# Optimization experiments

Measured on AMD Instinct MI355X. Metric: run time of the kernel, lower is better.

## Reference

```python
import jax, jax.numpy as jnp
import numpy as np
import math

B, S, D_IN, D_Q = 4, 2048, 512, 512

def setup_inputs() -> dict:
    key = jax.random.key(0)
    ks = jax.random.split(key, 7)
    s_in = 1.0 / math.sqrt(D_IN)
    x = jax.random.normal(ks[0], (B, S, D_IN), dtype=jnp.float32)
    # nn.Linear-style params: W [out,in], b [out]; uniform(-1/sqrt(in), 1/sqrt(in))
    Wq = jax.random.uniform(ks[1], (D_Q, D_IN), jnp.float32, -s_in, s_in)
    bq = jax.random.uniform(ks[2], (D_Q,), jnp.float32, -s_in, s_in)
    Wk = jax.random.uniform(ks[3], (D_Q, D_IN), jnp.float32, -s_in, s_in)
    bk = jax.random.uniform(ks[4], (D_Q,), jnp.float32, -s_in, s_in)
    Wv = jax.random.uniform(ks[5], (D_Q, D_IN), jnp.float32, -s_in, s_in)
    bv = jax.random.uniform(ks[6], (D_Q,), jnp.float32, -s_in, s_in)
    return {"x": x, "Wq": Wq, "bq": bq, "Wk": Wk, "bk": bk, "Wv": Wv, "bv": bv}

def reference(x, Wq, bq, Wk, bk, Wv, bv):
    # Q/K/V projections: [B,S,D_IN] @ W^T + b -> [B,S,D_Q]
    Q = jnp.einsum('bsi,qi->bsq', x, Wq) + bq
    K = jnp.einsum('bsi,qi->bsq', x, Wk) + bk
    V = jnp.einsum('bsi,qi->bsq', x, Wv) + bv
    scale = 1.0 / math.sqrt(D_Q)
    scores = jnp.einsum('bsq,btq->bst', Q, K) * scale  # [B,S,S]
    attention = jax.nn.softmax(scores, axis=-1)        # 'atten_prob'
    weighted = jnp.einsum('bst,btq->bsq', attention, V)  # 'atten_score'
    return (attention, weighted)
```

## Files before the change

### kernel.cpp

```cpp
#include <hip/hip_runtime.h>
#include <hip/hip_bf16.h>

typedef unsigned short u16;
typedef short bf16x8 __attribute__((ext_vector_type(8)));
typedef float f32x4 __attribute__((ext_vector_type(4)));

#define S_LEN 2048
#define DQ 512
#define NBATCH 4

__device__ __forceinline__ u16 f2bf(float f) {
    __hip_bfloat16 h = __float2bfloat16(f);
    return *reinterpret_cast<u16*>(&h);
}
__device__ __forceinline__ float bf2f(u16 u) {
    unsigned v = ((unsigned)u) << 16;
    union { unsigned u; float f; } c; c.u = v; return c.f;
}

__device__ __forceinline__ void async16(const u16* g, u16* l) {
    __builtin_amdgcn_global_load_lds(
        (__attribute__((address_space(1))) void*)g,
        (__attribute__((address_space(3))) void*)l, 16, 0, 0);
}

__device__ __forceinline__ int xcd_swz(int bid, int chunk) {
    return (bid & 7) * chunk + (bid >> 3);
}

__global__ __launch_bounds__(256) void k_cvt_all(const float* __restrict__ x,
                                                 const float* __restrict__ wq,
                                                 const float* __restrict__ wk,
                                                 const float* __restrict__ wv,
                                                 u16* __restrict__ xb, u16* __restrict__ wb) {
    int bid = blockIdx.x;
    const float* src;
    u16* dst;
    int i;
    if (bid < 4096)      { src = x;  dst = xb;          i = bid * 256 + threadIdx.x; }
    else if (bid < 4352) { src = wq; dst = wb;          i = (bid - 4096) * 256 + threadIdx.x; }
    else if (bid < 4608) { src = wk; dst = wb + 262144; i = (bid - 4352) * 256 + threadIdx.x; }
    else                 { src = wv; dst = wb + 524288; i = (bid - 4608) * 256 + threadIdx.x; }
    f32x4 v = *(const f32x4*)(src + (size_t)i * 4);
    ushort4 o;
    o.x = f2bf(v.x); o.y = f2bf(v.y); o.z = f2bf(v.z); o.w = f2bf(v.w);
    *(ushort4*)(dst + (size_t)i * 4) = o;
}

__device__ __forceinline__ void gemm_core(const u16* __restrict__ A, const u16* __restrict__ B,
                                          int lda, int ldb, int kend,
                                          f32x4 acc[4][4], u16* ldsA, u16* ldsB, int tid) {
    const int lane = tid & 63;
    const int w    = tid >> 6;
    const int wm   = (w & 1) << 6;
    const int wn   = (w >> 1) << 6;
    const int l16  = lane & 15;
    const int quad = lane >> 4;

    for (int k0 = 0; k0 < kend; k0 += 32) {
#pragma unroll
        for (int i = 0; i < 2; ++i) {
            int c  = i * 256 + tid;
            int r  = c >> 2;
            int cc = (c & 3) << 3;
            async16(A + (size_t)r * lda + k0 + cc, ldsA + r * 32 + cc);
            async16(B + (size_t)r * ldb + k0 + cc, ldsB + r * 32 + cc);
        }
        __syncthreads();
        bf16x8 af[4], bf[4];
#pragma unroll
        for (int i = 0; i < 4; ++i)
            af[i] = *(const bf16x8*)(ldsA + (wm + i * 16 + l16) * 32 + quad * 8);
#pragma unroll
        for (int j = 0; j < 4; ++j)
            bf[j] = *(const bf16x8*)(ldsB + (wn + j * 16 + l16) * 32 + quad * 8);
#pragma unroll
        for (int i = 0; i < 4; ++i)
#pragma unroll
            for (int j = 0; j < 4; ++j)
                acc[i][j] = __builtin_amdgcn_mfma_f32_16x16x32_bf16(af[i], bf[j], acc[i][j], 0, 0, 0);
        __syncthreads();
    }
}

__global__ __launch_bounds__(256) void k_proj(const u16* __restrict__ xb, const u16* __restrict__ Wb,
                                              const float* __restrict__ bq, const float* __restrict__ bk,
                                              const float* __restrict__ bv, u16* __restrict__ out,
                                              u16* __restrict__ VT) {
    __shared__ __align__(16) u16 lds[8192];
    const int l  = xcd_swz(blockIdx.x, 96);
    const int bx = l & 3;
    const int by = (l >> 2) & 63;
    const int z  = l >> 8;
    const int m0 = by * 128, n0 = bx * 128;
    const u16* A = xb + (size_t)m0 * DQ;
    const u16* B = Wb + (size_t)z * DQ * DQ + (size_t)n0 * DQ;
    const float* bias = (z == 0) ? bq : (z == 1) ? bk : bv;

    f32x4 acc[4][4];
#pragma unroll
    for (int i = 0; i < 4; ++i)
#pragma unroll
        for (int j = 0; j < 4; ++j) acc[i][j] = (f32x4)0.0f;

    int tid = threadIdx.x;
    gemm_core(A, B, DQ, DQ, DQ, acc, lds, lds + 4096, tid);

    const int lane = tid & 63, w = tid >> 6;
    const int wm = (w & 1) << 6, wn = (w >> 1) << 6;
    const int l16 = lane & 15, quad = lane >> 4;

    if (z < 2) {
        u16* outz = out + (size_t)z * 8192 * DQ;
#pragma unroll
        for (int j = 0; j < 4; ++j) {
            int gn = n0 + wn + j * 16 + l16;
            float bb = bias[gn];
#pragma unroll
            for (int i = 0; i < 4; ++i)
#pragma unroll
                for (int r = 0; r < 4; ++r) {
                    int gm = m0 + wm + i * 16 + quad * 4 + r;
                    outz[(size_t)gm * DQ + gn] = f2bf(acc[i][j][r] + bb);
                }
        }
    } else {
        const int b = m0 >> 11;
        u16* VTb_ = VT + (size_t)b * DQ * S_LEN;
#pragma unroll
        for (int j = 0; j < 4; ++j) {
            int gn = n0 + wn + j * 16 + l16;
            float bb = bias[gn];
#pragma unroll
            for (int i = 0; i < 4; ++i) {
                int t0 = (m0 & 2047) + wm + i * 16 + quad * 4;
                ushort4 o;
                o.x = f2bf(acc[i][j][0] + bb);
                o.y = f2bf(acc[i][j][1] + bb);
                o.z = f2bf(acc[i][j][2] + bb);
                o.w = f2bf(acc[i][j][3] + bb);
                *(ushort4*)(VTb_ + (size_t)gn * S_LEN + t0) = o;
            }
        }
    }
}

__global__ __launch_bounds__(256) void k_scores(const u16* __restrict__ Qb, const u16* __restrict__ Kb,
                                                u16* __restrict__ Pb) {
    __shared__ __align__(16) u16 lds[8192];
    const int l  = xcd_swz(blockIdx.x, 128);
    const int bx = l & 15;
    const int by = (l >> 4) & 15;
    const int b  = l >> 8;
    const int m0 = by * 128, n0 = bx * 128;
    const u16* A = Qb + ((size_t)b * S_LEN + m0) * DQ;
    const u16* B = Kb + ((size_t)b * S_LEN + n0) * DQ;

    f32x4 acc[4][4];
#pragma unroll
    for (int i = 0; i < 4; ++i)
#pragma unroll
        for (int j = 0; j < 4; ++j) acc[i][j] = (f32x4)0.0f;

    int tid = threadIdx.x;
    gemm_core(A, B, DQ, DQ, DQ, acc, lds, lds + 4096, tid);

    const float scale = 0.044194173824159216f;
    const int lane = tid & 63, w = tid >> 6;
    const int wm = (w & 1) << 6, wn = (w >> 1) << 6;
    const int l16 = lane & 15, quad = lane >> 4;
    u16* prow = Pb + (size_t)(b * S_LEN + m0) * S_LEN;
#pragma unroll
    for (int i = 0; i < 4; ++i)
#pragma unroll
        for (int j = 0; j < 4; ++j)
#pragma unroll
            for (int r = 0; r < 4; ++r) {
                int gm = wm + i * 16 + quad * 4 + r;
                int gn = n0 + wn + j * 16 + l16;
                prow[(size_t)gm * S_LEN + gn] = f2bf(__expf(acc[i][j][r] * scale));
            }
}

__global__ __launch_bounds__(256) void k_norm(const u16* __restrict__ Pb,
                                              float* __restrict__ probs,
                                              float* __restrict__ inv_sums) {
    __shared__ float red[4];
    const int row = blockIdx.x;
    const u16* pr = Pb + (size_t)row * S_LEN;
    float* outr = probs + (size_t)row * S_LEN;
    const int tid = threadIdx.x, lane = tid & 63, w = tid >> 6;

    bf16x8 pv = *(const bf16x8*)(pr + (size_t)tid * 8);
    float f[8];
#pragma unroll
    for (int k = 0; k < 8; ++k) f[k] = bf2f((u16)pv[k]);

    float sum = ((f[0] + f[1]) + (f[2] + f[3])) + ((f[4] + f[5]) + (f[6] + f[7]));
#pragma unroll
    for (int off = 32; off > 0; off >>= 1) sum += __shfl_xor(sum, off);
    if (lane == 0) red[w] = sum;
    __syncthreads();
    sum = (red[0] + red[1]) + (red[2] + red[3]);
    float inv = 1.0f / sum;
    if (tid == 0) inv_sums[row] = inv;

    f32x4 o0, o1;
    o0.x = f[0] * inv; o0.y = f[1] * inv; o0.z = f[2] * inv; o0.w = f[3] * inv;
    o1.x = f[4] * inv; o1.y = f[5] * inv; o1.z = f[6] * inv; o1.w = f[7] * inv;
    *(f32x4*)(outr + (size_t)tid * 8) = o0;
    *(f32x4*)(outr + (size_t)tid * 8 + 4) = o1;
}

__global__ __launch_bounds__(256) void k_pv(const u16* __restrict__ Pb, const u16* __restrict__ VT,
                                            const float* __restrict__ inv_sums,
                                            float* __restrict__ wout) {
    __shared__ __align__(16) u16 lds[12288];
    u16* ldsA = lds;
    u16* ldsB = lds + 8192;
    const int l  = xcd_swz(blockIdx.x, 64);
    const int bx = l & 7;
    const int by = (l >> 3) & 15;
    const int b  = l >> 7;
    const int m0 = by * 128, n0 = bx * 64;
    const u16* A = Pb + (size_t)(b * S_LEN + m0) * S_LEN;
    const u16* B = VT + (size_t)b * DQ * S_LEN + (size_t)n0 * S_LEN;

    const int tid  = threadIdx.x;
    const int lane = tid & 63;
    const int w    = tid >> 6;
    const int wm   = (w & 1) << 6;
    const int wn   = (w >> 1) << 5;
    const int l16  = lane & 15;
    const int quad = lane >> 4;

    f32x4 acc[4][2];
#pragma unroll
    for (int i = 0; i < 4; ++i)
#pragma unroll
        for (int j = 0; j < 2; ++j) acc[i][j] = (f32x4)0.0f;

    for (int k0 = 0; k0 < S_LEN; k0 += 64) {
#pragma unroll
        for (int h = 0; h < 2; ++h) {
#pragma unroll
            for (int it = 0; it < 2; ++it) {
                int c  = it * 256 + tid;
                int r  = c >> 2;
                int cc = (c & 3) << 3;
                async16(A + (size_t)r * S_LEN + k0 + h * 32 + cc, ldsA + h * 4096 + r * 32 + cc);
            }
            {
                int r  = tid >> 2;
                int cc = (tid & 3) << 3;
                async16(B + (size_t)r * S_LEN + k0 + h * 32 + cc, ldsB + h * 2048 + r * 32 + cc);
            }
        }
        __syncthreads();
        bf16x8 af[2][4], bfr[2][2];
#pragma unroll
        for (int h = 0; h < 2; ++h) {
#pragma unroll
            for (int i = 0; i < 4; ++i)
                af[h][i] = *(const bf16x8*)(ldsA + h * 4096 + (wm + i * 16 + l16) * 32 + quad * 8);
#pragma unroll
            for (int j = 0; j < 2; ++j)
                bfr[h][j] = *(const bf16x8*)(ldsB + h * 2048 + (wn + j * 16 + l16) * 32 + quad * 8);
        }
#pragma unroll
        for (int h = 0; h < 2; ++h)
#pragma unroll
            for (int i = 0; i < 4; ++i)
#pragma unroll
                for (int j = 0; j < 2; ++j)
                    acc[i][j] = __builtin_amdgcn_mfma_f32_16x16x32_bf16(af[h][i], bfr[h][j], acc[i][j], 0, 0, 0);
        __syncthreads();
    }

    const float* invb = inv_sums + b * S_LEN;
    float* outb = wout + (size_t)b * S_LEN * DQ;
#pragma unroll
    for (int i = 0; i < 4; ++i) {
#pragma unroll
        for (int r = 0; r < 4; ++r) {
            int gm = m0 + wm + i * 16 + quad * 4 + r;
            float inv = invb[gm];
#pragma unroll
            for (int j = 0; j < 2; ++j) {
                int gn = n0 + wn + j * 16 + l16;
                outb[(size_t)gm * DQ + gn] = acc[i][j][r] * inv;
            }
        }
    }
}

extern "C" void kernel_launch(void* const* d_in, const int* in_sizes, int n_in,
                              void* d_out, int out_size, void* d_ws, size_t ws_size,
                              hipStream_t stream) {
    const float* x  = (const float*)d_in[0];
    const float* Wq = (const float*)d_in[1];
    const float* bq = (const float*)d_in[2];
    const float* Wk = (const float*)d_in[3];
    const float* bk = (const float*)d_in[4];
    const float* Wv = (const float*)d_in[5];
    const float* bv = (const float*)d_in[6];

    char* ws = (char*)d_ws;
    u16* xb  = (u16*)(ws);
    u16* Wb  = (u16*)(ws + 8388608);
    u16* Qb  = (u16*)(ws + 9961472);
    u16* Kb  = (u16*)(ws + 18350080);
    u16* VTb = (u16*)(ws + 35127296);
    u16* Pb  = (u16*)(ws + 43515904);
    float* inv_sums = (float*)(ws + 77070336);
    float* probs = (float*)d_out;
    float* wout  = (float*)d_out + 16777216;

    k_cvt_all<<<4864, 256, 0, stream>>>(x, Wq, Wk, Wv, xb, Wb);
    k_proj<<<768, 256, 0, stream>>>(xb, Wb, bq, bk, bv, Qb, VTb);
    k_scores<<<1024, 256, 0, stream>>>(Qb, Kb, Pb);
    k_norm<<<8192, 256, 0, stream>>>(Pb, probs, inv_sums);
    k_pv<<<512, 256, 0, stream>>>(Pb, VTb, inv_sums, wout);
}
```

Before: 200.2 us.

## Fuse softmax normalization into scores and PV kernels, drop separate norm pass

Row sums of the exponentiated scores are now accumulated in the scores kernel through a wave shuffle reduction plus atomicAdd into a buffer that the convert kernel zeroes. The standalone normalization kernel is removed. The PV kernel writes the normalized fp32 probabilities from the P tile already staged in LDS, with each of the 8 column blocks handling its own 256-column slice. This avoids rereading the 32MB bf16 P matrix and one kernel launch, at the cost of atomics and extra global stores inside the PV main loop.

```diff
diff --git a/kernel.cpp b/kernel.cpp
--- a/kernel.cpp
+++ b/kernel.cpp
@@ -32,8 +32,14 @@
                                                  const float* __restrict__ wq,
                                                  const float* __restrict__ wk,
                                                  const float* __restrict__ wv,
-                                                 u16* __restrict__ xb, u16* __restrict__ wb) {
+                                                 u16* __restrict__ xb, u16* __restrict__ wb,
+                                                 float* __restrict__ sums) {
     int bid = blockIdx.x;
+    if (bid >= 4864) {
+        int i = (bid - 4864) * 256 + threadIdx.x;
+        *(f32x4*)(sums + (size_t)i * 4) = (f32x4)0.0f;
+        return;
+    }
     const float* src;
     u16* dst;
     int i;
@@ -146,7 +152,7 @@
 }
 
 __global__ __launch_bounds__(256) void k_scores(const u16* __restrict__ Qb, const u16* __restrict__ Kb,
-                                                u16* __restrict__ Pb) {
+                                                u16* __restrict__ Pb, float* __restrict__ sums) {
     __shared__ __align__(16) u16 lds[8192];
     const int l  = xcd_swz(blockIdx.x, 128);
     const int bx = l & 15;
@@ -170,6 +176,13 @@
     const int wm = (w & 1) << 6, wn = (w >> 1) << 6;
     const int l16 = lane & 15, quad = lane >> 4;
     u16* prow = Pb + (size_t)(b * S_LEN + m0) * S_LEN;
+
+    float psum[4][4];
+#pragma unroll
+    for (int i = 0; i < 4; ++i)
+#pragma unroll
+        for (int r = 0; r < 4; ++r) psum[i][r] = 0.0f;
+
 #pragma unroll
     for (int i = 0; i < 4; ++i)
 #pragma unroll
@@ -178,42 +191,29 @@
             for (int r = 0; r < 4; ++r) {
                 int gm = wm + i * 16 + quad * 4 + r;
                 int gn = n0 + wn + j * 16 + l16;
-                prow[(size_t)gm * S_LEN + gn] = f2bf(__expf(acc[i][j][r] * scale));
-            }
-}
-
-__global__ __launch_bounds__(256) void k_norm(const u16* __restrict__ Pb,
-                                              float* __restrict__ probs,
-                                              float* __restrict__ inv_sums) {
-    __shared__ float red[4];
-    const int row = blockIdx.x;
-    const u16* pr = Pb + (size_t)row * S_LEN;
-    float* outr = probs + (size_t)row * S_LEN;
-    const int tid = threadIdx.x, lane = tid & 63, w = tid >> 6;
-
-    bf16x8 pv = *(const bf16x8*)(pr + (size_t)tid * 8);
-    float f[8];
-#pragma unroll
-    for (int k = 0; k < 8; ++k) f[k] = bf2f((u16)pv[k]);
-
-    float sum = ((f[0] + f[1]) + (f[2] + f[3])) + ((f[4] + f[5]) + (f[6] + f[7]));
-#pragma unroll
-    for (int off = 32; off > 0; off >>= 1) sum += __shfl_xor(sum, off);
-    if (lane == 0) red[w] = sum;
-    __syncthreads();
-    sum = (red[0] + red[1]) + (red[2] + red[3]);
-    float inv = 1.0f / sum;
-    if (tid == 0) inv_sums[row] = inv;
-
-    f32x4 o0, o1;
-    o0.x = f[0] * inv; o0.y = f[1] * inv; o0.z = f[2] * inv; o0.w = f[3] * inv;
-    o1.x = f[4] * inv; o1.y = f[5] * inv; o1.z = f[6] * inv; o1.w = f[7] * inv;
-    *(f32x4*)(outr + (size_t)tid * 8) = o0;
-    *(f32x4*)(outr + (size_t)tid * 8 + 4) = o1;
+                float e = __expf(acc[i][j][r] * scale);
+                u16 pb = f2bf(e);
+                prow[(size_t)gm * S_LEN + gn] = pb;
+                psum[i][r] += bf2f(pb);
+            }
+
+    float* sums_row = sums + b * S_LEN + m0;
+#pragma unroll
+    for (int i = 0; i < 4; ++i)
+#pragma unroll
+        for (int r = 0; r < 4; ++r) {
+            float v = psum[i][r];
+            v += __shfl_xor(v, 1);
+            v += __shfl_xor(v, 2);
+            v += __shfl_xor(v, 4);
+            v += __shfl_xor(v, 8);
+            if (l16 == 0) atomicAdd(&sums_row[wm + i * 16 + quad * 4 + r], v);
+        }
 }
 
 __global__ __launch_bounds__(256) void k_pv(const u16* __restrict__ Pb, const u16* __restrict__ VT,
-                                            const float* __restrict__ inv_sums,
+                                            const float* __restrict__ sums,
+                                            float* __restrict__ probs,
                                             float* __restrict__ wout) {
     __shared__ __align__(16) u16 lds[12288];
     u16* ldsA = lds;
@@ -234,6 +234,11 @@
     const int l16  = lane & 15;
     const int quad = lane >> 4;
 
+    const int  pr_row = tid >> 1;
+    const int  pr_h   = tid & 1;
+    const float pr_inv = 1.0f / sums[b * S_LEN + m0 + pr_row];
+    float* probsb = probs + ((size_t)b * S_LEN + m0) * S_LEN;
+
     f32x4 acc[4][2];
 #pragma unroll
     for (int i = 0; i < 4; ++i)
@@ -274,17 +279,37 @@
 #pragma unroll
                 for (int j = 0; j < 2; ++j)
                     acc[i][j] = __builtin_amdgcn_mfma_f32_16x16x32_bf16(af[h][i], bfr[h][j], acc[i][j], 0, 0, 0);
+
+        if ((k0 >> 8) == bx) {
+            const u16* src = ldsA + pr_h * 4096 + pr_row * 32;
+            float* dst = probsb + (size_t)pr_row * S_LEN + k0 + pr_h * 32;
+#pragma unroll
+            for (int q = 0; q < 4; ++q) {
+                bf16x8 vv = *(const bf16x8*)(src + q * 8);
+                f32x4 o0, o1;
+                o0.x = bf2f((u16)vv[0]) * pr_inv;
+                o0.y = bf2f((u16)vv[1]) * pr_inv;
+                o0.z = bf2f((u16)vv[2]) * pr_inv;
+                o0.w = bf2f((u16)vv[3]) * pr_inv;
+                o1.x = bf2f((u16)vv[4]) * pr_inv;
+                o1.y = bf2f((u16)vv[5]) * pr_inv;
+                o1.z = bf2f((u16)vv[6]) * pr_inv;
+                o1.w = bf2f((u16)vv[7]) * pr_inv;
+                *(f32x4*)(dst + q * 8) = o0;
+                *(f32x4*)(dst + q * 8 + 4) = o1;
+            }
+        }
         __syncthreads();
     }
 
-    const float* invb = inv_sums + b * S_LEN;
+    const float* sumsb = sums + b * S_LEN;
     float* outb = wout + (size_t)b * S_LEN * DQ;
 #pragma unroll
     for (int i = 0; i < 4; ++i) {
 #pragma unroll
         for (int r = 0; r < 4; ++r) {
             int gm = m0 + wm + i * 16 + quad * 4 + r;
-            float inv = invb[gm];
+            float inv = 1.0f / sumsb[gm];
 #pragma unroll
             for (int j = 0; j < 2; ++j) {
                 int gn = n0 + wn + j * 16 + l16;
@@ -312,13 +337,12 @@
     u16* Kb  = (u16*)(ws + 18350080);
     u16* VTb = (u16*)(ws + 35127296);
     u16* Pb  = (u16*)(ws + 43515904);
-    float* inv_sums = (float*)(ws + 77070336);
+    float* sums = (float*)(ws + 77070336);
     float* probs = (float*)d_out;
     float* wout  = (float*)d_out + 16777216;
 
-    k_cvt_all<<<4864, 256, 0, stream>>>(x, Wq, Wk, Wv, xb, Wb);
+    k_cvt_all<<<4872, 256, 0, stream>>>(x, Wq, Wk, Wv, xb, Wb, sums);
     k_proj<<<768, 256, 0, stream>>>(xb, Wb, bq, bk, bv, Qb, VTb);
-    k_scores<<<1024, 256, 0, stream>>>(Qb, Kb, Pb);
-    k_norm<<<8192, 256, 0, stream>>>(Pb, probs, inv_sums);
-    k_pv<<<512, 256, 0, stream>>>(Pb, VTb, inv_sums, wout);
-}
+    k_scores<<<1024, 256, 0, stream>>>(Qb, Kb, Pb, sums);
+    k_pv<<<512, 256, 0, stream>>>(Pb, VTb, sums, probs, wout);
+}
```

After: 207.5 us. +3.6%, slower.
